# Performance work log

Measured on AMD Instinct MI355X. Metric: run time of the kernel, lower is better.

## Reference

```python
import jax, jax.numpy as jnp
import numpy as np
import math

D_MODEL = 1024
NHEAD = 16
HEAD_DIM = D_MODEL // NHEAD  # 64
R_HEAD = 8  # r // nhead = 128 // 16


def setup_inputs() -> dict:
    key = jax.random.key(0)
    ks = jax.random.split(key, 6)
    b, s = 2, 2048
    scale = 1.0 / math.sqrt(D_MODEL)
    return {
        "x": jax.random.normal(ks[0], (b, s, D_MODEL), dtype=jnp.float32),
        "Wq": jax.random.normal(ks[1], (D_MODEL, D_MODEL), dtype=jnp.float32) * scale,
        "Wk": jax.random.normal(ks[2], (D_MODEL, D_MODEL), dtype=jnp.float32) * scale,
        "Wv": jax.random.normal(ks[3], (D_MODEL, D_MODEL), dtype=jnp.float32) * scale,
        "Wo": jax.random.normal(ks[4], (D_MODEL, D_MODEL), dtype=jnp.float32) * scale,
        "B": jax.random.normal(ks[5], (D_MODEL, R_HEAD), dtype=jnp.float32),
    }


def reference(x, Wq, Wk, Wv, Wo, B):
    b, s, d = x.shape
    # Linear projections (torch nn.Linear: y = x @ W.T)
    Q = (x @ Wq.T).reshape(b, s, NHEAD, HEAD_DIM).transpose(0, 2, 1, 3)  # [b,h,s,hd]
    K = (x @ Wk.T).reshape(b, s, NHEAD, HEAD_DIM).transpose(0, 2, 1, 3)
    V = (x @ Wv.T).reshape(b, s, NHEAD, HEAD_DIM).transpose(0, 2, 1, 3)
    # Shared basis: head h uses rows [h*head_dim : (h+1)*head_dim] of B
    B_heads = B.reshape(NHEAD, HEAD_DIM, R_HEAD)  # [h,hd,r]
    # Low-rank projected queries/keys (vectorized form of the per-head loop)
    Qr = jnp.einsum('bhsd,hdr->bhsr', Q, B_heads)  # [b,h,s,r]
    Kr = jnp.einsum('bhsd,hdr->bhsr', K, B_heads)
    scores = jnp.einsum('bhqr,bhkr->bhqk', Qr, Kr) / math.sqrt(R_HEAD)  # [b,h,s,s]
    attn = jax.nn.softmax(scores, axis=-1)  # dropout is identity in eval
    out = jnp.einsum('bhqk,bhkd->bhqd', attn, V)  # [b,h,s,hd]
    out = out.transpose(0, 2, 1, 3).reshape(b, s, d)
    return out @ Wo.T
```

## Files before the change

kernel.cpp:

```cpp
#include <hip/hip_runtime.h>

#define SEQ 2048
#define DM 1024

typedef __attribute__((ext_vector_type(8))) short bs8;
typedef __attribute__((ext_vector_type(4))) float vf4;
typedef __attribute__((ext_vector_type(4))) unsigned int vu4;

__device__ __forceinline__ unsigned short bf16u(float f) {
  unsigned int u = __float_as_uint(f);
  u = (u + 0x7fffu + ((u >> 16) & 1u)) >> 16;
  return (unsigned short)u;
}

__device__ __forceinline__ unsigned int cvt_pk(float lo, float hi) {
  unsigned int r;
  asm("v_cvt_pk_bf16_f32 %0, %1, %2" : "=v"(r) : "v"(lo), "v"(hi));
  return r;
}

__device__ __forceinline__ float fexp2(float x) {
  float r;
  asm("v_exp_f32 %0, %1" : "=v"(r) : "v"(x));
  return r;
}

__device__ __forceinline__ void gload16(const unsigned short* g, unsigned short* l) {
  __builtin_amdgcn_global_load_lds(
      (const __attribute__((address_space(1))) unsigned int*)g,
      (__attribute__((address_space(3))) unsigned int*)l, 16, 0, 0);
}

__global__ void k_combine(const float* __restrict__ Wq, const float* __restrict__ Wk,
                          const float* __restrict__ Bm,
                          unsigned short* __restrict__ Ch, unsigned short* __restrict__ Cl) {
  int e = blockIdx.x * 256 + threadIdx.x;
  int which = e >> 17;
  int rem = e & 131071;
  int hr = rem >> 10;
  int j = rem & 1023;
  int h = hr >> 3, r = hr & 7;
  const float* W = which ? Wk : Wq;
  float acc = 0.f;
  #pragma unroll 8
  for (int d = 0; d < 64; d++) {
    int gd = h * 64 + d;
    acc += Bm[gd * 8 + r] * W[gd * 1024 + j];
  }
  size_t idx = (size_t)(which * 128 + hr) * 1024 + j;
  unsigned short h16 = bf16u(acc);
  float hf = __uint_as_float(((unsigned int)h16) << 16);
  Ch[idx] = h16;
  Cl[idx] = bf16u(acc - hf);
}

__global__ void k_cvt(const float* __restrict__ in, unsigned short* __restrict__ out, int n4) {
  int i = blockIdx.x * 256 + threadIdx.x;
  if (i >= n4) return;
  float4 v = ((const float4*)in)[i];
  ushort4 o;
  o.x = bf16u(v.x); o.y = bf16u(v.y); o.z = bf16u(v.z); o.w = bf16u(v.w);
  ((ushort4*)out)[i] = o;
}

__global__ void k_cvt_hl(const float* __restrict__ in, unsigned short* __restrict__ oh,
                         unsigned short* __restrict__ ol, int n4) {
  int i = blockIdx.x * 256 + threadIdx.x;
  if (i >= n4) return;
  float4 v = ((const float4*)in)[i];
  float f[4] = {v.x, v.y, v.z, v.w};
  ushort4 hv, lv;
  unsigned short hs[4], ls[4];
  #pragma unroll
  for (int j = 0; j < 4; j++) {
    unsigned short h16 = bf16u(f[j]);
    float hf = __uint_as_float(((unsigned int)h16) << 16);
    hs[j] = h16;
    ls[j] = bf16u(f[j] - hf);
  }
  hv.x = hs[0]; hv.y = hs[1]; hv.z = hs[2]; hv.w = hs[3];
  lv.x = ls[0]; lv.y = ls[1]; lv.z = ls[2]; lv.w = ls[3];
  ((ushort4*)oh)[i] = hv;
  ((ushort4*)ol)[i] = lv;
}

__global__ __launch_bounds__(256) void k_qkr(
    const unsigned short* __restrict__ Xh, const unsigned short* __restrict__ Xl,
    const unsigned short* __restrict__ Bh_, const unsigned short* __restrict__ Bl_,
    float* __restrict__ C0, float* __restrict__ C1) {
  const int K = 1024, N = 256;
  __shared__ unsigned short Sah[64 * 64];
  __shared__ unsigned short Sal[64 * 64];
  __shared__ unsigned short Sbh[64 * 64];
  __shared__ unsigned short Sbl[64 * 64];
  int t = threadIdx.x, lane = t & 63, w = t >> 6;
  int gg = lane >> 4, r = lane & 15;
  int m0 = blockIdx.x * 64, n0 = blockIdx.y * 64;
  int kz = blockIdx.z;
  float* C = kz ? C1 : C0;
  vf4 acc[4];
  #pragma unroll
  for (int fn = 0; fn < 4; fn++) acc[fn] = (vf4){0.f, 0.f, 0.f, 0.f};

  int prow = lane >> 3, pslot = lane & 7;
  const unsigned short *ah_src[2], *al_src[2], *bh_src[2], *bl_src[2];
  unsigned short *ah_dst[2], *al_dst[2], *bh_dst[2], *bl_dst[2];
  #pragma unroll
  for (int p = 0; p < 2; p++) {
    int rr = w * 16 + p * 8 + prow;
    int c = pslot ^ ((rr ^ (rr >> 3)) & 7);
    size_t ga = (size_t)(m0 + rr) * K + (size_t)kz * 512 + c * 8;
    ah_src[p] = Xh + ga;  al_src[p] = Xl + ga;
    size_t gb = (size_t)(n0 + rr) * K + (size_t)kz * 512 + c * 8;
    bh_src[p] = Bh_ + gb; bl_src[p] = Bl_ + gb;
    int ldo = (w * 16 + p * 8) * 64;
    ah_dst[p] = &Sah[ldo]; al_dst[p] = &Sal[ldo];
    bh_dst[p] = &Sbh[ldo]; bl_dst[p] = &Sbl[ldo];
  }

  int aoff[2], boff[4][2];
  {
    int arow = w * 16 + r;
    int key = (arow ^ (arow >> 3)) & 7;
    #pragma unroll
    for (int kk = 0; kk < 2; kk++) aoff[kk] = arow * 64 + ((kk * 4 + gg) ^ key) * 8;
  }
  #pragma unroll
  for (int fn = 0; fn < 4; fn++) {
    int brow = fn * 16 + r;
    int key = (brow ^ (brow >> 3)) & 7;
    #pragma unroll
    for (int kk = 0; kk < 2; kk++) boff[fn][kk] = brow * 64 + ((kk * 4 + gg) ^ key) * 8;
  }

  for (int k0 = 0; k0 < 512; k0 += 64) {
    __syncthreads();
    #pragma unroll
    for (int p = 0; p < 2; p++) {
      gload16(ah_src[p] + k0, ah_dst[p]);
      gload16(al_src[p] + k0, al_dst[p]);
      gload16(bh_src[p] + k0, bh_dst[p]);
      gload16(bl_src[p] + k0, bl_dst[p]);
    }
    __syncthreads();
    bs8 afh[2], afl[2], bfh[4][2], bfl[4][2];
    #pragma unroll
    for (int kk = 0; kk < 2; kk++) {
      afh[kk] = *(const bs8*)&Sah[aoff[kk]];
      afl[kk] = *(const bs8*)&Sal[aoff[kk]];
    }
    #pragma unroll
    for (int fn = 0; fn < 4; fn++)
      #pragma unroll
      for (int kk = 0; kk < 2; kk++) {
        bfh[fn][kk] = *(const bs8*)&Sbh[boff[fn][kk]];
        bfl[fn][kk] = *(const bs8*)&Sbl[boff[fn][kk]];
      }
    #pragma unroll
    for (int kk = 0; kk < 2; kk++)
      #pragma unroll
      for (int fn = 0; fn < 4; fn++) {
        acc[fn] = __builtin_amdgcn_mfma_f32_16x16x32_bf16(afh[kk], bfh[fn][kk], acc[fn], 0, 0, 0);
        acc[fn] = __builtin_amdgcn_mfma_f32_16x16x32_bf16(afh[kk], bfl[fn][kk], acc[fn], 0, 0, 0);
        acc[fn] = __builtin_amdgcn_mfma_f32_16x16x32_bf16(afl[kk], bfh[fn][kk], acc[fn], 0, 0, 0);
      }
  }

  #pragma unroll
  for (int fn = 0; fn < 4; fn++)
    #pragma unroll
    for (int j = 0; j < 4; j++) {
      int m = m0 + w * 16 + gg * 4 + j;
      int n = n0 + fn * 16 + r;
      C[(size_t)m * N + n] = acc[fn][j];
    }
}

__global__ void k_hilo(const float* __restrict__ QA, const float* __restrict__ QB,
                       unsigned short* __restrict__ Qhl, unsigned short* __restrict__ Khl) {
  int i = blockIdx.x * 256 + threadIdx.x;
  int side = i >> 16;
  int nh = i & 65535;
  int n = nh & 4095;
  int h = nh >> 12;
  size_t off = (size_t)n * 256 + side * 128 + h * 8;
  const float sc = side ? 1.0f : (1.4426950408889634f * 0.35355339059327373f);
  unsigned short* dst = (side ? Khl : Qhl) + ((size_t)h * 4096 + n) * 16;
  float4 a0 = *(const float4*)&QA[off];
  float4 a1 = *(const float4*)&QA[off + 4];
  float4 b0 = *(const float4*)&QB[off];
  float4 b1 = *(const float4*)&QB[off + 4];
  float f[8] = {a0.x+b0.x, a0.y+b0.y, a0.z+b0.z, a0.w+b0.w,
                a1.x+b1.x, a1.y+b1.y, a1.z+b1.z, a1.w+b1.w};
  unsigned short hs[8], ls[8];
  #pragma unroll
  for (int j = 0; j < 8; j++) {
    float fs = f[j] * sc;
    unsigned short h16 = bf16u(fs);
    float hf = __uint_as_float(((unsigned int)h16) << 16);
    hs[j] = h16;
    ls[j] = bf16u(fs - hf);
  }
  uint4 hv = {(unsigned int)hs[0] | ((unsigned int)hs[1] << 16),
              (unsigned int)hs[2] | ((unsigned int)hs[3] << 16),
              (unsigned int)hs[4] | ((unsigned int)hs[5] << 16),
              (unsigned int)hs[6] | ((unsigned int)hs[7] << 16)};
  uint4 lv = {(unsigned int)ls[0] | ((unsigned int)ls[1] << 16),
              (unsigned int)ls[2] | ((unsigned int)ls[3] << 16),
              (unsigned int)ls[4] | ((unsigned int)ls[5] << 16),
              (unsigned int)ls[6] | ((unsigned int)ls[7] << 16)};
  *(uint4*)dst = hv;
  *(uint4*)(dst + 8) = lv;
}

template<int OUT>
__global__ __launch_bounds__(256) void k_gemm128(const unsigned short* __restrict__ A,
    const unsigned short* __restrict__ W, void* __restrict__ Cout, int M, int N, int K) {
  __shared__ unsigned short Ah[128 * 64];
  __shared__ unsigned short Bh[64 * 64];
  int t = threadIdx.x, lane = t & 63, w = t >> 6;
  int gg = lane >> 4, r = lane & 15;
  int m0 = blockIdx.x * 128, n0 = blockIdx.y * 64;
  vf4 acc[2][4];
  #pragma unroll
  for (int i = 0; i < 2; i++)
    #pragma unroll
    for (int j = 0; j < 4; j++) acc[i][j] = (vf4){0.f, 0.f, 0.f, 0.f};

  int prow = lane >> 3, pslot = lane & 7;
  const unsigned short* asrc[4];
  unsigned short* aldst[4];
  #pragma unroll
  for (int p = 0; p < 4; p++) {
    int rr = w * 32 + p * 8 + prow;
    int c = pslot ^ ((rr ^ (rr >> 3)) & 7);
    asrc[p] = &A[(size_t)(m0 + rr) * K + c * 8];
    aldst[p] = &Ah[(w * 32 + p * 8) * 64];
  }
  const unsigned short* bsrc[2];
  unsigned short* bldst[2];
  #pragma unroll
  for (int p = 0; p < 2; p++) {
    int rn = w * 16 + p * 8 + prow;
    int c = pslot ^ ((rn ^ (rn >> 3)) & 7);
    bsrc[p] = &W[(size_t)(n0 + rn) * K + c * 8];
    bldst[p] = &Bh[(w * 16 + p * 8) * 64];
  }

  int aoff[2][2], boff[4][2];
  #pragma unroll
  for (int fm = 0; fm < 2; fm++) {
    int arow = w * 32 + fm * 16 + r;
    int key = (arow ^ (arow >> 3)) & 7;
    #pragma unroll
    for (int kk = 0; kk < 2; kk++)
      aoff[fm][kk] = arow * 64 + ((kk * 4 + gg) ^ key) * 8;
  }
  #pragma unroll
  for (int fn = 0; fn < 4; fn++) {
    int brow = fn * 16 + r;
    int key = (brow ^ (brow >> 3)) & 7;
    #pragma unroll
    for (int kk = 0; kk < 2; kk++)
      boff[fn][kk] = brow * 64 + ((kk * 4 + gg) ^ key) * 8;
  }

  for (int k0 = 0; k0 < K; k0 += 64) {
    __syncthreads();
    #pragma unroll
    for (int p = 0; p < 4; p++) gload16(asrc[p] + k0, aldst[p]);
    #pragma unroll
    for (int p = 0; p < 2; p++) gload16(bsrc[p] + k0, bldst[p]);
    __syncthreads();
    bs8 af[2][2], bf[4][2];
    #pragma unroll
    for (int fm = 0; fm < 2; fm++)
      #pragma unroll
      for (int kk = 0; kk < 2; kk++) af[fm][kk] = *(const bs8*)&Ah[aoff[fm][kk]];
    #pragma unroll
    for (int fn = 0; fn < 4; fn++)
      #pragma unroll
      for (int kk = 0; kk < 2; kk++) bf[fn][kk] = *(const bs8*)&Bh[boff[fn][kk]];
    #pragma unroll
    for (int kk = 0; kk < 2; kk++)
      #pragma unroll
      for (int fm = 0; fm < 2; fm++)
        #pragma unroll
        for (int fn = 0; fn < 4; fn++)
          acc[fm][fn] = __builtin_amdgcn_mfma_f32_16x16x32_bf16(af[fm][kk], bf[fn][kk], acc[fm][fn], 0, 0, 0);
  }

  #pragma unroll
  for (int fm = 0; fm < 2; fm++)
    #pragma unroll
    for (int fn = 0; fn < 4; fn++) {
      if (OUT == 2) {
        int n = n0 + fn * 16 + r;
        int m = m0 + w * 32 + fm * 16 + gg * 4;
        ushort4 st = {bf16u(acc[fm][fn][0]), bf16u(acc[fm][fn][1]),
                      bf16u(acc[fm][fn][2]), bf16u(acc[fm][fn][3])};
        *(ushort4*)&((unsigned short*)Cout)[(size_t)n * M + m] = st;
      } else {
        #pragma unroll
        for (int j = 0; j < 4; j++) {
          int m = m0 + w * 32 + fm * 16 + gg * 4 + j;
          int n = n0 + fn * 16 + r;
          ((float*)Cout)[(size_t)m * N + n] = acc[fm][fn][j];
        }
      }
    }
}

__global__ __launch_bounds__(256, 8) void k_attn(const unsigned short* __restrict__ Qhl,
    const unsigned short* __restrict__ Khl, const unsigned short* __restrict__ Vt,
    unsigned short* __restrict__ AO) {
  int bx = blockIdx.x;
  int qt = bx & 63, h = (bx >> 6) & 15, b = bx >> 10;
  int t = threadIdx.x, lane = t & 63, w = t >> 6;
  int wq = w & 1, kvg = w >> 1;
  int gg = lane >> 4, r = lane & 15;

  __shared__ unsigned short VT[2][4096];

  int qglob = b * 2048 + qt * 32 + wq * 16 + r;
  bs8 bq = {0, 0, 0, 0, 0, 0, 0, 0};
  if (gg != 3)
    bq = *(const bs8*)&Qhl[((size_t)h * 4096 + qglob) * 16 + (gg == 2 ? 8 : 0)];

  const unsigned short* Khead = &Khl[((size_t)h * 4096 + (size_t)b * 2048 + (size_t)kvg * 1024) * 16];
  int koff = (gg == 1) ? 8 : 0;
  int ks0 = (r >> 2) * 8 + (r & 3);
  const unsigned short* kp0 = Khead + (size_t)ks0 * 16 + koff;

  int srow = lane >> 3, sslot = lane & 7;
  const unsigned short* vsrc[4];
  unsigned short* vdst[4];
  #pragma unroll
  for (int c = 0; c < 4; c++) {
    int d = wq * 32 + c * 8 + srow;
    int key = (d ^ (d >> 2)) & 7;
    vsrc[c] = &Vt[(size_t)(h * 64 + d) * 4096 + (size_t)b * 2048 + (size_t)kvg * 1024
                  + (size_t)(sslot ^ key) * 8];
    vdst[c] = &VT[kvg][(wq * 32 + c * 8) * 64];
  }

  int pvoff[2][4];
  #pragma unroll
  for (int sl = 0; sl < 2; sl++)
    #pragma unroll
    for (int fn = 0; fn < 4; fn++) {
      int row = 4 * r + fn;
      int key = (row ^ (row >> 2)) & 7;
      pvoff[sl][fn] = row * 64 + ((sl * 4 + gg) ^ key) * 8;
    }

  float mrun = -INFINITY;
  vf4 acc[4];
  #pragma unroll
  for (int i = 0; i < 4; i++) acc[i] = (vf4){0.f, 0.f, 0.f, 0.f};
  vf4 accs = (vf4){0.f, 0.f, 0.f, 0.f};

  const bs8 ones = (bs8){16256, 16256, 16256, 16256, 16256, 16256, 16256, 16256};

  for (int kc = 0; kc < 16; kc++) {
    size_t kb = (size_t)kc * 1024;
    bs8 af0 = *(const bs8*)(kp0 + kb);
    bs8 af1 = *(const bs8*)(kp0 + kb + 32 * 16);
    bs8 af2 = *(const bs8*)(kp0 + kb + 4 * 16);
    bs8 af3 = *(const bs8*)(kp0 + kb + 36 * 16);

    __syncthreads();
    #pragma unroll
    for (int c = 0; c < 4; c++) gload16(vsrc[c] + kc * 64, vdst[c]);
    __syncthreads();

    vf4 z = (vf4){0.f, 0.f, 0.f, 0.f};
    __builtin_amdgcn_s_setprio(1);
    vf4 s0 = __builtin_amdgcn_mfma_f32_16x16x32_bf16(af0, bq, z, 0, 0, 0);
    vf4 s1 = __builtin_amdgcn_mfma_f32_16x16x32_bf16(af1, bq, z, 0, 0, 0);
    vf4 s2 = __builtin_amdgcn_mfma_f32_16x16x32_bf16(af2, bq, z, 0, 0, 0);
    vf4 s3 = __builtin_amdgcn_mfma_f32_16x16x32_bf16(af3, bq, z, 0, 0, 0);
    __builtin_amdgcn_s_setprio(0);

    float p[16];
    #pragma unroll
    for (int j = 0; j < 4; j++) {
      p[0 + j] = s0[j]; p[4 + j] = s1[j]; p[8 + j] = s2[j]; p[12 + j] = s3[j];
    }
    float cm0 = fmaxf(fmaxf(p[0],  p[1]),  p[2]);
    float cm1 = fmaxf(fmaxf(p[3],  p[4]),  p[5]);
    float cm2 = fmaxf(fmaxf(p[6],  p[7]),  p[8]);
    float cm3 = fmaxf(fmaxf(p[9],  p[10]), p[11]);
    float cm4 = fmaxf(fmaxf(p[12], p[13]), p[14]);
    float cmax = fmaxf(fmaxf(fmaxf(cm0, cm1), cm2),
                       fmaxf(fmaxf(cm3, cm4), p[15]));
    cmax = fmaxf(cmax, __shfl_xor(cmax, 16));
    cmax = fmaxf(cmax, __shfl_xor(cmax, 32));

    if (!__all(cmax <= mrun + 8.f)) {
      float mnew = fmaxf(mrun, cmax);
      float alpha = fexp2(mrun - mnew);
      float al[4];
      #pragma unroll
      for (int j = 0; j < 4; j++) al[j] = __shfl(alpha, gg * 4 + j);
      #pragma unroll
      for (int fn = 0; fn < 4; fn++) {
        acc[fn][0] *= al[0]; acc[fn][1] *= al[1];
        acc[fn][2] *= al[2]; acc[fn][3] *= al[3];
      }
      accs[0] *= al[0]; accs[1] *= al[1];
      accs[2] *= al[2]; accs[3] *= al[3];
      mrun = mnew;
    }

    #pragma unroll
    for (int i = 0; i < 16; i++) p[i] = fexp2(p[i] - mrun);

    vu4 a0 = {cvt_pk(p[0],  p[1]),  cvt_pk(p[2],  p[3]),
              cvt_pk(p[8],  p[9]),  cvt_pk(p[10], p[11])};
    vu4 a1 = {cvt_pk(p[4],  p[5]),  cvt_pk(p[6],  p[7]),
              cvt_pk(p[12], p[13]), cvt_pk(p[14], p[15])};
    bs8 apv0 = __builtin_bit_cast(bs8, a0);
    bs8 apv1 = __builtin_bit_cast(bs8, a1);

    const unsigned short* vb = &VT[kvg][0];
    __builtin_amdgcn_s_setprio(1);
    #pragma unroll
    for (int sl = 0; sl < 2; sl++) {
      bs8 a = sl ? apv1 : apv0;
      #pragma unroll
      for (int fn = 0; fn < 4; fn++) {
        bs8 bv = *(const bs8*)&vb[pvoff[sl][fn]];
        acc[fn] = __builtin_amdgcn_mfma_f32_16x16x32_bf16(a, bv, acc[fn], 0, 0, 0);
      }
    }
    accs = __builtin_amdgcn_mfma_f32_16x16x32_bf16(apv0, ones, accs, 0, 0, 0);
    accs = __builtin_amdgcn_mfma_f32_16x16x32_bf16(apv1, ones, accs, 0, 0, 0);
    __builtin_amdgcn_s_setprio(0);
  }

  __syncthreads();
  float* Lm = (float*)&VT[0][0];
  float* Ll = Lm + 32;
  float* La = Lm + 64;
  if (kvg == 1) {
    if (gg == 0) Lm[wq * 16 + r] = mrun;
    if (r == 0) {
      #pragma unroll
      for (int j = 0; j < 4; j++) Ll[wq * 16 + gg * 4 + j] = accs[j];
    }
    float* dst = &La[(wq * 64 + lane) * 20];
    #pragma unroll
    for (int fn = 0; fn < 4; fn++) *(vf4*)(dst + fn * 4) = acc[fn];
  }
  __syncthreads();
  if (kvg == 1) return;

  float m1 = Lm[wq * 16 + r];
  float mx = fmaxf(mrun, m1);
  float e0 = fexp2(mrun - mx), e1 = fexp2(m1 - mx);
  float al0[4], al1[4], l1[4];
  #pragma unroll
  for (int j = 0; j < 4; j++) {
    al0[j] = __shfl(e0, gg * 4 + j);
    al1[j] = __shfl(e1, gg * 4 + j);
    l1[j] = Ll[wq * 16 + gg * 4 + j];
  }
  const float* src = &La[(wq * 64 + lane) * 20];
  #pragma unroll
  for (int fn = 0; fn < 4; fn++) {
    vf4 o1 = *(const vf4*)(src + fn * 4);
    #pragma unroll
    for (int j = 0; j < 4; j++)
      acc[fn][j] = acc[fn][j] * al0[j] + o1[j] * al1[j];
  }
  #pragma unroll
  for (int j = 0; j < 4; j++) accs[j] = accs[j] * al0[j] + l1[j] * al1[j];

  float li[4];
  #pragma unroll
  for (int j = 0; j < 4; j++) li[j] = 1.f / accs[j];
  #pragma unroll
  for (int j = 0; j < 4; j++) {
    uint2 o;
    o.x = cvt_pk(acc[0][j] * li[j], acc[1][j] * li[j]);
    o.y = cvt_pk(acc[2][j] * li[j], acc[3][j] * li[j]);
    int qq = qt * 32 + wq * 16 + gg * 4 + j;
    *(uint2*)&AO[((size_t)b * SEQ + qq) * 1024 + h * 64 + 4 * r] = o;
  }
}

extern "C" void kernel_launch(void* const* d_in, const int* in_sizes, int n_in,
                              void* d_out, int out_size, void* d_ws, size_t ws_size,
                              hipStream_t stream) {
  const float* x  = (const float*)d_in[0];
  const float* Wq = (const float*)d_in[1];
  const float* Wk = (const float*)d_in[2];
  const float* Wv = (const float*)d_in[3];
  const float* Wo = (const float*)d_in[4];
  const float* Bm = (const float*)d_in[5];
  float* out = (float*)d_out;

  char* ws = (char*)d_ws;
  unsigned short* Cqkh = (unsigned short*)ws;  ws += (size_t)256 * 1024 * 2;
  unsigned short* Cqkl = (unsigned short*)ws;  ws += (size_t)256 * 1024 * 2;
  float* QKrA = (float*)ws;                    ws += (size_t)4096 * 256 * 4;
  float* QKrB = (float*)ws;                    ws += (size_t)4096 * 256 * 4;
  unsigned short* xh  = (unsigned short*)ws;   ws += (size_t)4096 * 1024 * 2;
  unsigned short* Wvh = (unsigned short*)ws;   ws += (size_t)1024 * 1024 * 2;
  unsigned short* Woh = (unsigned short*)ws;   ws += (size_t)1024 * 1024 * 2;
  unsigned short* Vt  = (unsigned short*)ws;   ws += (size_t)4096 * 1024 * 2;
  unsigned short* AO  = (unsigned short*)ws;   ws += (size_t)4096 * 1024 * 2;
  unsigned short* Qhl = (unsigned short*)ws;   ws += (size_t)16 * 4096 * 16 * 2;
  unsigned short* Khl = (unsigned short*)ws;   ws += (size_t)16 * 4096 * 16 * 2;
  unsigned short* xl = AO;

  k_combine<<<1024, 256, 0, stream>>>(Wq, Wk, Bm, Cqkh, Cqkl);
  k_cvt_hl<<<4096, 256, 0, stream>>>(x, xh, xl, 1048576);
  k_cvt<<<1024, 256, 0, stream>>>(Wv, Wvh, 262144);
  k_cvt<<<1024, 256, 0, stream>>>(Wo, Woh, 262144);
  k_qkr<<<dim3(64, 4, 2), 256, 0, stream>>>(xh, xl, Cqkh, Cqkl, QKrA, QKrB);
  k_hilo<<<512, 256, 0, stream>>>(QKrA, QKrB, Qhl, Khl);
  k_gemm128<2><<<dim3(32, 16), 256, 0, stream>>>(xh, Wvh, (void*)Vt, 4096, 1024, 1024);
  k_attn<<<2048, 256, 0, stream>>>(Qhl, Khl, Vt, AO);
  k_gemm128<0><<<dim3(32, 16), 256, 0, stream>>>(AO, Woh, (void*)out, 4096, 1024, 1024);
}
```

Measured before the change: 146.0 us.

## Fuse low-rank QK projection with hi/lo split, drop split-K partial buffers

Replaces the split-K projection kernel and the separate hi/lo conversion kernel with a single kernel. It uses 32-row tiles over the full K dimension and stages the fp32 result through shared memory, then writes bf16 hi/lo Q and K directly. This removes the fp32 partial buffers, their round trip through global memory and one launch. In exchange each block runs a longer K loop with smaller tiles. The attention kernel also switches to 32-bit offsets and lowers its launch-bounds occupancy hint from 8 to 6.

Result: faster. 122.8 us (-15.8%).

```diff
diff --git a/kernel.cpp b/kernel.cpp
--- a/kernel.cpp
+++ b/kernel.cpp
@@ -84,118 +84,104 @@
   ((ushort4*)ol)[i] = lv;
 }
 
-__global__ __launch_bounds__(256) void k_qkr(
+__global__ __launch_bounds__(256) void k_qkr2(
     const unsigned short* __restrict__ Xh, const unsigned short* __restrict__ Xl,
     const unsigned short* __restrict__ Bh_, const unsigned short* __restrict__ Bl_,
-    float* __restrict__ C0, float* __restrict__ C1) {
-  const int K = 1024, N = 256;
-  __shared__ unsigned short Sah[64 * 64];
-  __shared__ unsigned short Sal[64 * 64];
-  __shared__ unsigned short Sbh[64 * 64];
-  __shared__ unsigned short Sbl[64 * 64];
+    unsigned short* __restrict__ Qhl, unsigned short* __restrict__ Khl) {
+  const int K = 1024;
+  __shared__ unsigned short SS[12288];
+  unsigned short* Ah = SS;
+  unsigned short* Al = SS + 2048;
+  unsigned short* Bh = SS + 4096;
+  unsigned short* Bl = SS + 8192;
   int t = threadIdx.x, lane = t & 63, w = t >> 6;
   int gg = lane >> 4, r = lane & 15;
-  int m0 = blockIdx.x * 64, n0 = blockIdx.y * 64;
-  int kz = blockIdx.z;
-  float* C = kz ? C1 : C0;
-  vf4 acc[4];
-  #pragma unroll
-  for (int fn = 0; fn < 4; fn++) acc[fn] = (vf4){0.f, 0.f, 0.f, 0.f};
+  int wm = w & 1, wn = w >> 1;
+  int m0 = blockIdx.x * 32, n0 = blockIdx.y * 64;
+  vf4 acc[2];
+  #pragma unroll
+  for (int fn = 0; fn < 2; fn++) acc[fn] = (vf4){0.f, 0.f, 0.f, 0.f};
 
   int prow = lane >> 3, pslot = lane & 7;
-  const unsigned short *ah_src[2], *al_src[2], *bh_src[2], *bl_src[2];
-  unsigned short *ah_dst[2], *al_dst[2], *bh_dst[2], *bl_dst[2];
+  int arl = w * 8 + prow;
+  int akey = (arl ^ (arl >> 3)) & 7;
+  const unsigned short* ah_src = Xh + (size_t)(m0 + arl) * K + (pslot ^ akey) * 8;
+  const unsigned short* al_src = Xl + (size_t)(m0 + arl) * K + (pslot ^ akey) * 8;
+  unsigned short* ah_dst = &Ah[(w * 8) * 64];
+  unsigned short* al_dst = &Al[(w * 8) * 64];
+  const unsigned short *bh_src[2], *bl_src[2];
+  unsigned short *bh_dst[2], *bl_dst[2];
   #pragma unroll
   for (int p = 0; p < 2; p++) {
-    int rr = w * 16 + p * 8 + prow;
-    int c = pslot ^ ((rr ^ (rr >> 3)) & 7);
-    size_t ga = (size_t)(m0 + rr) * K + (size_t)kz * 512 + c * 8;
-    ah_src[p] = Xh + ga;  al_src[p] = Xl + ga;
-    size_t gb = (size_t)(n0 + rr) * K + (size_t)kz * 512 + c * 8;
-    bh_src[p] = Bh_ + gb; bl_src[p] = Bl_ + gb;
-    int ldo = (w * 16 + p * 8) * 64;
-    ah_dst[p] = &Sah[ldo]; al_dst[p] = &Sal[ldo];
-    bh_dst[p] = &Sbh[ldo]; bl_dst[p] = &Sbl[ldo];
-  }
-
-  int aoff[2], boff[4][2];
+    int brl = w * 16 + p * 8 + prow;
+    int bkey = (brl ^ (brl >> 3)) & 7;
+    bh_src[p] = Bh_ + (size_t)(n0 + brl) * K + (pslot ^ bkey) * 8;
+    bl_src[p] = Bl_ + (size_t)(n0 + brl) * K + (pslot ^ bkey) * 8;
+    bh_dst[p] = &Bh[(w * 16 + p * 8) * 64];
+    bl_dst[p] = &Bl[(w * 16 + p * 8) * 64];
+  }
+
+  int aoff[2], boff[2][2];
   {
-    int arow = w * 16 + r;
+    int arow = wm * 16 + r;
     int key = (arow ^ (arow >> 3)) & 7;
     #pragma unroll
     for (int kk = 0; kk < 2; kk++) aoff[kk] = arow * 64 + ((kk * 4 + gg) ^ key) * 8;
   }
   #pragma unroll
-  for (int fn = 0; fn < 4; fn++) {
-    int brow = fn * 16 + r;
+  for (int fn = 0; fn < 2; fn++) {
+    int brow = wn * 32 + fn * 16 + r;
     int key = (brow ^ (brow >> 3)) & 7;
     #pragma unroll
     for (int kk = 0; kk < 2; kk++) boff[fn][kk] = brow * 64 + ((kk * 4 + gg) ^ key) * 8;
   }
 
-  for (int k0 = 0; k0 < 512; k0 += 64) {
+  for (int k0 = 0; k0 < K; k0 += 64) {
     __syncthreads();
+    gload16(ah_src + k0, ah_dst);
+    gload16(al_src + k0, al_dst);
     #pragma unroll
     for (int p = 0; p < 2; p++) {
-      gload16(ah_src[p] + k0, ah_dst[p]);
-      gload16(al_src[p] + k0, al_dst[p]);
       gload16(bh_src[p] + k0, bh_dst[p]);
       gload16(bl_src[p] + k0, bl_dst[p]);
     }
     __syncthreads();
-    bs8 afh[2], afl[2], bfh[4][2], bfl[4][2];
+    bs8 afh[2], afl[2];
     #pragma unroll
     for (int kk = 0; kk < 2; kk++) {
-      afh[kk] = *(const bs8*)&Sah[aoff[kk]];
-      afl[kk] = *(const bs8*)&Sal[aoff[kk]];
-    }
-    #pragma unroll
-    for (int fn = 0; fn < 4; fn++)
-      #pragma unroll
-      for (int kk = 0; kk < 2; kk++) {
-        bfh[fn][kk] = *(const bs8*)&Sbh[boff[fn][kk]];
-        bfl[fn][kk] = *(const bs8*)&Sbl[boff[fn][kk]];
+      afh[kk] = *(const bs8*)&Ah[aoff[kk]];
+      afl[kk] = *(const bs8*)&Al[aoff[kk]];
+    }
+    #pragma unroll
+    for (int kk = 0; kk < 2; kk++)
+      #pragma unroll
+      for (int fn = 0; fn < 2; fn++) {
+        bs8 bfh = *(const bs8*)&Bh[boff[fn][kk]];
+        bs8 bfl = *(const bs8*)&Bl[boff[fn][kk]];
+        acc[fn] = __builtin_amdgcn_mfma_f32_16x16x32_bf16(afh[kk], bfh, acc[fn], 0, 0, 0);
+        acc[fn] = __builtin_amdgcn_mfma_f32_16x16x32_bf16(afh[kk], bfl, acc[fn], 0, 0, 0);
+        acc[fn] = __builtin_amdgcn_mfma_f32_16x16x32_bf16(afl[kk], bfh, acc[fn], 0, 0, 0);
       }
-    #pragma unroll
-    for (int kk = 0; kk < 2; kk++)
-      #pragma unroll
-      for (int fn = 0; fn < 4; fn++) {
-        acc[fn] = __builtin_amdgcn_mfma_f32_16x16x32_bf16(afh[kk], bfh[fn][kk], acc[fn], 0, 0, 0);
-        acc[fn] = __builtin_amdgcn_mfma_f32_16x16x32_bf16(afh[kk], bfl[fn][kk], acc[fn], 0, 0, 0);
-        acc[fn] = __builtin_amdgcn_mfma_f32_16x16x32_bf16(afl[kk], bfh[fn][kk], acc[fn], 0, 0, 0);
-      }
-  }
-
-  #pragma unroll
-  for (int fn = 0; fn < 4; fn++)
-    #pragma unroll
-    for (int j = 0; j < 4; j++) {
-      int m = m0 + w * 16 + gg * 4 + j;
-      int n = n0 + fn * 16 + r;
-      C[(size_t)m * N + n] = acc[fn][j];
-    }
-}
-
-__global__ void k_hilo(const float* __restrict__ QA, const float* __restrict__ QB,
-                       unsigned short* __restrict__ Qhl, unsigned short* __restrict__ Khl) {
-  int i = blockIdx.x * 256 + threadIdx.x;
-  int side = i >> 16;
-  int nh = i & 65535;
-  int n = nh & 4095;
-  int h = nh >> 12;
-  size_t off = (size_t)n * 256 + side * 128 + h * 8;
+  }
+
+  __syncthreads();
+  float* Sc = (float*)SS;
+  #pragma unroll
+  for (int fn = 0; fn < 2; fn++)
+    #pragma unroll
+    for (int j = 0; j < 4; j++)
+      Sc[(wm * 16 + gg * 4 + j) * 65 + wn * 32 + fn * 16 + r] = acc[fn][j];
+  __syncthreads();
+
+  int g = t >> 5, xr = t & 31;
+  const float* srcrow = &Sc[xr * 65 + g * 8];
+  int side = (n0 >= 128) ? 1 : 0;
+  int hh = ((n0 & 127) >> 3) + g;
   const float sc = side ? 1.0f : (1.4426950408889634f * 0.35355339059327373f);
-  unsigned short* dst = (side ? Khl : Qhl) + ((size_t)h * 4096 + n) * 16;
-  float4 a0 = *(const float4*)&QA[off];
-  float4 a1 = *(const float4*)&QA[off + 4];
-  float4 b0 = *(const float4*)&QB[off];
-  float4 b1 = *(const float4*)&QB[off + 4];
-  float f[8] = {a0.x+b0.x, a0.y+b0.y, a0.z+b0.z, a0.w+b0.w,
-                a1.x+b1.x, a1.y+b1.y, a1.z+b1.z, a1.w+b1.w};
   unsigned short hs[8], ls[8];
   #pragma unroll
   for (int j = 0; j < 8; j++) {
-    float fs = f[j] * sc;
+    float fs = srcrow[j] * sc;
     unsigned short h16 = bf16u(fs);
     float hf = __uint_as_float(((unsigned int)h16) << 16);
     hs[j] = h16;
@@ -209,6 +195,7 @@
               (unsigned int)ls[2] | ((unsigned int)ls[3] << 16),
               (unsigned int)ls[4] | ((unsigned int)ls[5] << 16),
               (unsigned int)ls[6] | ((unsigned int)ls[7] << 16)};
+  unsigned short* dst = (side ? Khl : Qhl) + ((size_t)hh * 4096 + (m0 + xr)) * 16;
   *(uint4*)dst = hv;
   *(uint4*)(dst + 8) = lv;
 }
@@ -311,7 +298,7 @@
     }
 }
 
-__global__ __launch_bounds__(256, 8) void k_attn(const unsigned short* __restrict__ Qhl,
+__global__ __launch_bounds__(256, 6) void k_attn(const unsigned short* __restrict__ Qhl,
     const unsigned short* __restrict__ Khl, const unsigned short* __restrict__ Vt,
     unsigned short* __restrict__ AO) {
   int bx = blockIdx.x;
@@ -327,21 +314,17 @@
   if (gg != 3)
     bq = *(const bs8*)&Qhl[((size_t)h * 4096 + qglob) * 16 + (gg == 2 ? 8 : 0)];
 
-  const unsigned short* Khead = &Khl[((size_t)h * 4096 + (size_t)b * 2048 + (size_t)kvg * 1024) * 16];
-  int koff = (gg == 1) ? 8 : 0;
-  int ks0 = (r >> 2) * 8 + (r & 3);
-  const unsigned short* kp0 = Khead + (size_t)ks0 * 16 + koff;
+  unsigned int kbase = ((unsigned int)(h * 4096 + b * 2048 + kvg * 1024
+                        + (r >> 2) * 8 + (r & 3)) << 4) + ((gg == 1) ? 8u : 0u);
 
   int srow = lane >> 3, sslot = lane & 7;
-  const unsigned short* vsrc[4];
-  unsigned short* vdst[4];
+  unsigned int voff[4];
   #pragma unroll
   for (int c = 0; c < 4; c++) {
     int d = wq * 32 + c * 8 + srow;
     int key = (d ^ (d >> 2)) & 7;
-    vsrc[c] = &Vt[(size_t)(h * 64 + d) * 4096 + (size_t)b * 2048 + (size_t)kvg * 1024
-                  + (size_t)(sslot ^ key) * 8];
-    vdst[c] = &VT[kvg][(wq * 32 + c * 8) * 64];
+    voff[c] = (unsigned int)((h * 64 + d) * 4096 + b * 2048 + kvg * 1024
+                             + (sslot ^ key) * 8);
   }
 
   int pvoff[2][4];
@@ -363,15 +346,16 @@
   const bs8 ones = (bs8){16256, 16256, 16256, 16256, 16256, 16256, 16256, 16256};
 
   for (int kc = 0; kc < 16; kc++) {
-    size_t kb = (size_t)kc * 1024;
-    bs8 af0 = *(const bs8*)(kp0 + kb);
-    bs8 af1 = *(const bs8*)(kp0 + kb + 32 * 16);
-    bs8 af2 = *(const bs8*)(kp0 + kb + 4 * 16);
-    bs8 af3 = *(const bs8*)(kp0 + kb + 36 * 16);
+    const unsigned short* kpc = Khl + kbase + (unsigned int)(kc * 1024);
+    bs8 af0 = *(const bs8*)(kpc);
+    bs8 af1 = *(const bs8*)(kpc + 512);
+    bs8 af2 = *(const bs8*)(kpc + 64);
+    bs8 af3 = *(const bs8*)(kpc + 576);
 
     __syncthreads();
     #pragma unroll
-    for (int c = 0; c < 4; c++) gload16(vsrc[c] + kc * 64, vdst[c]);
+    for (int c = 0; c < 4; c++)
+      gload16(Vt + voff[c] + (unsigned int)(kc * 64), &VT[kvg][(wq * 32 + c * 8) * 64]);
     __syncthreads();
 
     vf4 z = (vf4){0.f, 0.f, 0.f, 0.f};
@@ -504,8 +488,6 @@
   char* ws = (char*)d_ws;
   unsigned short* Cqkh = (unsigned short*)ws;  ws += (size_t)256 * 1024 * 2;
   unsigned short* Cqkl = (unsigned short*)ws;  ws += (size_t)256 * 1024 * 2;
-  float* QKrA = (float*)ws;                    ws += (size_t)4096 * 256 * 4;
-  float* QKrB = (float*)ws;                    ws += (size_t)4096 * 256 * 4;
   unsigned short* xh  = (unsigned short*)ws;   ws += (size_t)4096 * 1024 * 2;
   unsigned short* Wvh = (unsigned short*)ws;   ws += (size_t)1024 * 1024 * 2;
   unsigned short* Woh = (unsigned short*)ws;   ws += (size_t)1024 * 1024 * 2;
@@ -519,8 +501,7 @@
   k_cvt_hl<<<4096, 256, 0, stream>>>(x, xh, xl, 1048576);
   k_cvt<<<1024, 256, 0, stream>>>(Wv, Wvh, 262144);
   k_cvt<<<1024, 256, 0, stream>>>(Wo, Woh, 262144);
-  k_qkr<<<dim3(64, 4, 2), 256, 0, stream>>>(xh, xl, Cqkh, Cqkl, QKrA, QKrB);
-  k_hilo<<<512, 256, 0, stream>>>(QKrA, QKrB, Qhl, Khl);
+  k_qkr2<<<dim3(128, 4), 256, 0, stream>>>(xh, xl, Cqkh, Cqkl, Qhl, Khl);
   k_gemm128<2><<<dim3(32, 16), 256, 0, stream>>>(xh, Wvh, (void*)Vt, 4096, 1024, 1024);
   k_attn<<<2048, 256, 0, stream>>>(Qhl, Khl, Vt, AO);
   k_gemm128<0><<<dim3(32, 16), 256, 0, stream>>>(AO, Woh, (void*)out, 4096, 1024, 1024);
```
